# Kernel optimization log

Hardware: AMD Instinct MI355X
Metric: run time of the kernel (lower is better)

## Reference

```python
import jax, jax.numpy as jnp
import numpy as np

B, N, K, D, H = 32, 4096, 8, 256, 512
ITERS = 3
LN_EPS = 1e-5  # torch LayerNorm default; self.eps is unused in forward


def _ln(x, g, b):
    m = jnp.mean(x, axis=-1, keepdims=True)
    v = jnp.mean(jnp.square(x - m), axis=-1, keepdims=True)
    return (x - m) * jax.lax.rsqrt(v + LN_EPS) * g + b


def setup_inputs() -> dict:
    key = jax.random.key(0)
    ks = jax.random.split(key, 16)
    s = 0.02
    return {
        "inputs": jax.random.normal(ks[0], (B, N, D), jnp.float32),
        "slots_init": jax.random.normal(ks[1], (B, K, D), jnp.float32),
        "ln_in_g": jnp.ones((D,), jnp.float32), "ln_in_b": jnp.zeros((D,), jnp.float32),
        "ln_s_g": jnp.ones((D,), jnp.float32), "ln_s_b": jnp.zeros((D,), jnp.float32),
        "ln_ff_g": jnp.ones((D,), jnp.float32), "ln_ff_b": jnp.zeros((D,), jnp.float32),
        "Wk": s * jax.random.normal(ks[2], (D, D), jnp.float32), "bk": jnp.zeros((D,), jnp.float32),
        "Wq": s * jax.random.normal(ks[3], (D, D), jnp.float32), "bq": jnp.zeros((D,), jnp.float32),
        "Wv": s * jax.random.normal(ks[4], (D, D), jnp.float32), "bv": jnp.zeros((D,), jnp.float32),
        "W_ih": s * jax.random.normal(ks[5], (3 * D, D), jnp.float32),
        "b_ih": jnp.zeros((3 * D,), jnp.float32),
        "W_hh": s * jax.random.normal(ks[6], (3 * D, D), jnp.float32),
        "b_hh": jnp.zeros((3 * D,), jnp.float32),
        "W1": s * jax.random.normal(ks[7], (H, D), jnp.float32), "b1": jnp.zeros((H,), jnp.float32),
        "W2": s * jax.random.normal(ks[8], (D, H), jnp.float32), "b2": jnp.zeros((D,), jnp.float32),
    }


def _gru_cell(x, h, W_ih, b_ih, W_hh, b_hh):
    # PyTorch GRUCell: gates in order r, z, n
    gi = x @ W_ih.T + b_ih  # [*, 3D]
    gh = h @ W_hh.T + b_hh
    ir, iz, inn = jnp.split(gi, 3, axis=-1)
    hr, hz, hn = jnp.split(gh, 3, axis=-1)
    r = jax.nn.sigmoid(ir + hr)
    z = jax.nn.sigmoid(iz + hz)
    n = jnp.tanh(inn + r * hn)
    return (1.0 - z) * n + z * h


def reference(inputs, slots_init, ln_in_g, ln_in_b, ln_s_g, ln_s_b, ln_ff_g, ln_ff_b,
              Wk, bk, Wq, bq, Wv, bv, W_ih, b_ih, W_hh, b_hh, W1, b1, W2, b2):
    d = inputs.shape[-1]
    x = _ln(inputs, ln_in_g, ln_in_b)  # [B,N,D]
    # k, v depend only on x; hoisted out of the loop (same math as source)
    k = x @ Wk.T + bk                  # project_inputs
    v = x @ Wv.T + bv                  # project_v
    scale = 1.0 / jnp.sqrt(jnp.asarray(d, inputs.dtype))
    slots = slots_init
    for _ in range(ITERS):
        slots_prev = slots
        q = _ln(slots, ln_s_g, ln_s_b) @ Wq.T + bq          # [B,K,D]
        attn_logits = jnp.einsum('bkd,bnd->bkn', q, k) * scale
        # competitive softmax over the SLOT axis (dim=1), not keys
        attn = jax.nn.softmax(attn_logits, axis=1)          # [B,K,N]
        updates = jnp.einsum('bkn,bnd->bkd', attn, v)
        slots = _gru_cell(updates, slots_prev, W_ih, b_ih, W_hh, b_hh)
        hdd = jax.nn.relu(_ln(slots, ln_ff_g, ln_ff_b) @ W1.T + b1)
        slots = slots + hdd @ W2.T + b2
    return slots
```

## Files before the change

kernel.cpp:

```cpp
#include <hip/hip_runtime.h>
#include <hip/hip_bf16.h>
#include <cstddef>
#include <cstdint>

#define BB 32
#define NN 4096
#define KK 8
#define DD 256
#define HH 512
#define LN_EPS 1e-5f
#define SCALE 0.0625f
#define NCHUNK 32

__device__ __forceinline__ float wave_sum(float v) {
#pragma unroll
  for (int off = 32; off >= 1; off >>= 1) v += __shfl_xor(v, off);
  return v;
}

__device__ __forceinline__ float sigmoidf_(float x) { return 1.0f / (1.0f + __expf(-x)); }

#define OFF_G   0
#define OFF_W1  393216
#define OFF_W2  524288
#define OFF_WV  655360
#define OFF_WQ  720896
#define OFF_WK  786432
#define WB_ELEMS 851968

#define G_PRE (BB * KK)
#define G_W2B (512 * 11)
#define G_SETUP (G_PRE + G_W2B)

__device__ __forceinline__ float dotp4(uint2 w, float4 s) {
  return __uint_as_float(w.x << 16) * s.x + __uint_as_float(w.x & 0xffff0000u) * s.y +
         __uint_as_float(w.y << 16) * s.z + __uint_as_float(w.y & 0xffff0000u) * s.w;
}

template <int OUT, int KL>
__device__ __forceinline__ float gemv_p(const ushort* __restrict__ wt, int j, int kb,
                                        const float* __restrict__ src) {
  const uint2* p = (const uint2*)(wt + ((size_t)(kb >> 2) * OUT + j) * 4);
  float a = 0.0f;
#pragma unroll 16
  for (int e = 0; e < KL / 4; ++e) {
    uint2 w = p[(size_t)e * OUT];
    float4 s = *(const float4*)(src + kb + e * 4);
    a += dotp4(w, s);
  }
  return a;
}

__global__ __launch_bounds__(256) void k_setup(
    const float* __restrict__ Wih, const float* __restrict__ Whh,
    const float* __restrict__ W1, const float* __restrict__ W2,
    const float* __restrict__ Wv, const float* __restrict__ Wq,
    const float* __restrict__ Wk, ushort* __restrict__ wb,
    const float* __restrict__ slots, const float* __restrict__ gs, const float* __restrict__ bs,
    const float* __restrict__ bq, const float* __restrict__ bk,
    float* __restrict__ qk, float* __restrict__ qb) {
  int blk = blockIdx.x;
  if (blk < G_PRE) {
    int row = blk;
    int t = threadIdx.x;
    int wid = t >> 6, lane = t & 63;
    __shared__ float lns[DD];
    __shared__ float qs[DD];
    __shared__ float rb[8];
    float sv = slots[(size_t)row * DD + t];
    float s = wave_sum(sv);
    float s2 = wave_sum(sv * sv);
    if (lane == 0) { rb[wid] = s; rb[4 + wid] = s2; }
    __syncthreads();
    float tot = rb[0] + rb[1] + rb[2] + rb[3];
    float tot2 = rb[4] + rb[5] + rb[6] + rb[7];
    float m = tot * (1.0f / DD);
    float var = tot2 * (1.0f / DD) - m * m;
    float rs = rsqrtf(var + LN_EPS);
    lns[t] = (sv - m) * rs * gs[t] + bs[t];
    __syncthreads();
    float acc = 0.0f;
    const float4* wr = (const float4*)(Wq + (size_t)t * DD);
#pragma unroll 4
    for (int e4 = 0; e4 < DD / 4; ++e4) {
      float4 w = wr[e4];
      float4 l = ((const float4*)lns)[e4];
      acc += w.x * l.x + w.y * l.y + w.z * l.z + w.w * l.w;
    }
    qs[t] = acc + bq[t];
    __syncthreads();
    float a2 = 0.0f;
    for (int d = 0; d < DD; ++d) a2 = fmaf(qs[d], Wk[(size_t)d * DD + t], a2);
    qk[(size_t)row * DD + t] = SCALE * a2;
    float pb = wave_sum(qs[t] * bk[t]);
    __syncthreads();
    if (lane == 0) rb[wid] = pb;
    __syncthreads();
    if (t == 0) qb[row] = SCALE * (rb[0] + rb[1] + rb[2] + rb[3]);
  } else {
    int q2 = blk - G_PRE;
    int m = q2 >> 9;
    int idx = (q2 & 511) * 256 + threadIdx.x;
    const int sizes[11] = {65536, 65536, 65536, 65536, 65536, 65536, 131072, 131072, 65536, 65536, 65536};
    const int offs[11] = {OFF_G, OFF_G + 65536, OFF_G + 131072, OFF_G + 196608, OFF_G + 262144,
                          OFF_G + 327680, OFF_W1, OFF_W2, OFF_WV, OFF_WQ, OFF_WK};
    if (idx >= sizes[m]) return;
    int K = (m == 7) ? 512 : 256;
    int OUT = (m == 6) ? 512 : 256;
    int k = idx % K, j = idx / K;
    float v;
    switch (m) {
      case 0: case 1: case 2: v = Wih[((size_t)(m * 256 + j)) * 256 + k]; break;
      case 3: case 4: case 5: v = Whh[((size_t)((m - 3) * 256 + j)) * 256 + k]; break;
      case 6: v = W1[(size_t)j * 256 + k]; break;
      case 7: v = W2[(size_t)j * 512 + k]; break;
      case 8: v = Wv[(size_t)j * 256 + k]; break;
      case 9: v = Wq[(size_t)j * 256 + k]; break;
      default: v = Wk[(size_t)k * 256 + j]; break;
    }
    __hip_bfloat16 h = __float2bfloat16(v);
    wb[(size_t)offs[m] + (size_t)(k >> 2) * OUT * 4 + j * 4 + (k & 3)] = *(ushort*)&h;
  }
}

template <int DO_LN>
__global__ __launch_bounds__(256) void k_attn_t(const ushort* __restrict__ xb_in,
                                                ushort* __restrict__ xb_out,
                                                const float* __restrict__ inp,
                                                const float* __restrict__ lg,
                                                const float* __restrict__ lb,
                                                const float* __restrict__ qk,
                                                const float* __restrict__ qb,
                                                float* __restrict__ uxp,
                                                float* __restrict__ sap) {
  int wid = threadIdx.x >> 6, lane = threadIdx.x & 63;
  int wg = blockIdx.x * 4 + wid;
  int b = wg >> 7, wc = wg & 127;
  int l32 = lane & 31, half = lane >> 5;
  int d0 = l32 * 8;
  __shared__ float bx[KK][DD];
  __shared__ float sred[4][KK];
  float4 qa[8], qc[8];
  {
    const float* base = qk + (size_t)b * (KK * DD) + d0;
#pragma unroll
    for (int k = 0; k < 8; ++k) {
      qa[k] = *(const float4*)(base + k * DD);
      qc[k] = *(const float4*)(base + k * DD + 4);
    }
  }
  int km = ((lane & 1) << 2) | (lane & 2) | ((lane >> 2) & 1);
  float qb_mine = qb[b * 8 + km];
  float g8[8], b8[8];
  const float* rp;
  ushort* wp;
  const uint4* px;
  uint4 xv;
  if (DO_LN) {
#pragma unroll
    for (int j = 0; j < 8; ++j) { g8[j] = lg[d0 + j]; b8[j] = lb[d0 + j]; }
    rp = inp + ((size_t)b * NN + wc * 32 + half) * DD + d0;
    wp = xb_out + ((size_t)b * NN + wc * 32 + half) * DD + d0;
  } else {
    px = (const uint4*)(xb_in + ((size_t)b * NN + wc * 32 + half) * DD + d0);
    xv = px[0];
  }
  float4 ac0[8] = {}, ac1[8] = {};
  float sacc = 0.0f;
#pragma unroll 2
  for (int it = 0; it < 16; ++it) {
    float xf[8];
    if (DO_LN) {
      float4 v0 = *(const float4*)rp;
      float4 v1 = *(const float4*)(rp + 4);
      float s = v0.x + v0.y + v0.z + v0.w + v1.x + v1.y + v1.z + v1.w;
      float s2 = v0.x * v0.x + v0.y * v0.y + v0.z * v0.z + v0.w * v0.w +
                 v1.x * v1.x + v1.y * v1.y + v1.z * v1.z + v1.w * v1.w;
#pragma unroll
      for (int off = 16; off >= 1; off >>= 1) {
        s += __shfl_xor(s, off);
        s2 += __shfl_xor(s2, off);
      }
      float m = s * (1.0f / DD);
      float var = s2 * (1.0f / DD) - m * m;
      float rs = rsqrtf(var + LN_EPS);
      xf[0] = (v0.x - m) * rs * g8[0] + b8[0];
      xf[1] = (v0.y - m) * rs * g8[1] + b8[1];
      xf[2] = (v0.z - m) * rs * g8[2] + b8[2];
      xf[3] = (v0.w - m) * rs * g8[3] + b8[3];
      xf[4] = (v1.x - m) * rs * g8[4] + b8[4];
      xf[5] = (v1.y - m) * rs * g8[5] + b8[5];
      xf[6] = (v1.z - m) * rs * g8[6] + b8[6];
      xf[7] = (v1.w - m) * rs * g8[7] + b8[7];
      uint4 st;
      {
        __hip_bfloat16 h0 = __float2bfloat16(xf[0]), h1 = __float2bfloat16(xf[1]);
        __hip_bfloat16 h2 = __float2bfloat16(xf[2]), h3 = __float2bfloat16(xf[3]);
        __hip_bfloat16 h4 = __float2bfloat16(xf[4]), h5 = __float2bfloat16(xf[5]);
        __hip_bfloat16 h6 = __float2bfloat16(xf[6]), h7 = __float2bfloat16(xf[7]);
        st.x = (uint)*(ushort*)&h0 | ((uint)*(ushort*)&h1 << 16);
        st.y = (uint)*(ushort*)&h2 | ((uint)*(ushort*)&h3 << 16);
        st.z = (uint)*(ushort*)&h4 | ((uint)*(ushort*)&h5 << 16);
        st.w = (uint)*(ushort*)&h6 | ((uint)*(ushort*)&h7 << 16);
      }
      *(uint4*)wp = st;
      rp += 2 * DD;
      wp += 2 * DD;
    } else {
      uint4 nx = (it < 15) ? px[(size_t)(it + 1) * 64] : xv;
      xf[0] = __uint_as_float(xv.x << 16); xf[1] = __uint_as_float(xv.x & 0xffff0000u);
      xf[2] = __uint_as_float(xv.y << 16); xf[3] = __uint_as_float(xv.y & 0xffff0000u);
      xf[4] = __uint_as_float(xv.z << 16); xf[5] = __uint_as_float(xv.z & 0xffff0000u);
      xf[6] = __uint_as_float(xv.w << 16); xf[7] = __uint_as_float(xv.w & 0xffff0000u);
      xv = nx;
    }
    float l[8];
#pragma unroll
    for (int k = 0; k < 8; ++k) {
      l[k] = xf[0] * qa[k].x + xf[1] * qa[k].y + xf[2] * qa[k].z + xf[3] * qa[k].w +
             xf[4] * qc[k].x + xf[5] * qc[k].y + xf[6] * qc[k].z + xf[7] * qc[k].w;
    }
#pragma unroll
    for (int i = 0; i < 4; ++i) {
      float keep = (lane & 1) ? l[i + 4] : l[i];
      float send = (lane & 1) ? l[i] : l[i + 4];
      l[i] = keep + __shfl_xor(send, 1);
    }
#pragma unroll
    for (int i = 0; i < 2; ++i) {
      float keep = (lane & 2) ? l[i + 2] : l[i];
      float send = (lane & 2) ? l[i] : l[i + 2];
      l[i] = keep + __shfl_xor(send, 2);
    }
    {
      float keep = (lane & 4) ? l[1] : l[0];
      float send = (lane & 4) ? l[0] : l[1];
      l[0] = keep + __shfl_xor(send, 4);
    }
    float lv = l[0] + __shfl_xor(l[0], 8);
    lv += __shfl_xor(lv, 16);
    lv += qb_mine;
    float mx = fmaxf(lv, __shfl_xor(lv, 1));
    mx = fmaxf(mx, __shfl_xor(mx, 2));
    mx = fmaxf(mx, __shfl_xor(mx, 4));
    float p = __expf(lv - mx);
    float ss = p + __shfl_xor(p, 1);
    ss += __shfl_xor(ss, 2);
    ss += __shfl_xor(ss, 4);
    float a = p * __frcp_rn(ss);
    sacc += a;
    float ga[8];
    ga[0] = a;
    ga[1] = __shfl_xor(ga[0], 1);
    ga[2] = __shfl_xor(ga[0], 2);
    ga[3] = __shfl_xor(ga[1], 2);
    ga[4] = __shfl_xor(ga[0], 4);
    ga[5] = __shfl_xor(ga[1], 4);
    ga[6] = __shfl_xor(ga[2], 4);
    ga[7] = __shfl_xor(ga[3], 4);
#pragma unroll
    for (int j = 0; j < 8; ++j) {
      float aj = ga[j];
      ac0[j].x = fmaf(aj, xf[0], ac0[j].x);
      ac0[j].y = fmaf(aj, xf[1], ac0[j].y);
      ac0[j].z = fmaf(aj, xf[2], ac0[j].z);
      ac0[j].w = fmaf(aj, xf[3], ac0[j].w);
      ac1[j].x = fmaf(aj, xf[4], ac1[j].x);
      ac1[j].y = fmaf(aj, xf[5], ac1[j].y);
      ac1[j].z = fmaf(aj, xf[6], ac1[j].z);
      ac1[j].w = fmaf(aj, xf[7], ac1[j].w);
    }
  }
#pragma unroll
  for (int j = 0; j < 8; ++j) {
    ac0[j].x += __shfl_xor(ac0[j].x, 32);
    ac0[j].y += __shfl_xor(ac0[j].y, 32);
    ac0[j].z += __shfl_xor(ac0[j].z, 32);
    ac0[j].w += __shfl_xor(ac0[j].w, 32);
    ac1[j].x += __shfl_xor(ac1[j].x, 32);
    ac1[j].y += __shfl_xor(ac1[j].y, 32);
    ac1[j].z += __shfl_xor(ac1[j].z, 32);
    ac1[j].w += __shfl_xor(ac1[j].w, 32);
  }
  sacc += __shfl_xor(sacc, 32);
  if (lane < 8) sred[wid][km] = sacc;
#pragma unroll
  for (int w = 0; w < 4; ++w) {
    if (wid == w && half == 0) {
#pragma unroll
      for (int j = 0; j < 8; ++j) {
        int lx = (l32 ^ j) & 7;
        int kj = ((lx & 1) << 2) | (lx & 2) | ((lx >> 2) & 1);
        float4* p0 = (float4*)&bx[kj][d0];
        float4* p1 = (float4*)&bx[kj][d0 + 4];
        if (w == 0) {
          *p0 = ac0[j];
          *p1 = ac1[j];
        } else {
          float4 c0 = *p0, c1 = *p1;
          c0.x += ac0[j].x; c0.y += ac0[j].y; c0.z += ac0[j].z; c0.w += ac0[j].w;
          c1.x += ac1[j].x; c1.y += ac1[j].y; c1.z += ac1[j].z; c1.w += ac1[j].w;
          *p0 = c0; *p1 = c1;
        }
      }
    }
    __syncthreads();
  }
  int bb2 = blockIdx.x >> 5, c = blockIdx.x & 31;
  {
    int t = threadIdx.x;
    int k = t >> 5, dd = (t & 31) * 8;
    float* dst = uxp + (((size_t)(bb2 * NCHUNK + c)) * KK + k) * DD + dd;
    *(float4*)dst = *(float4*)&bx[k][dd];
    *(float4*)(dst + 4) = *(float4*)&bx[k][dd + 4];
    if (t < 8)
      sap[((size_t)(bb2 * NCHUNK + c)) * KK + t] =
          sred[0][t] + sred[1][t] + sred[2][t] + sred[3][t];
  }
}

__global__ __launch_bounds__(1024) void k_fused(const float* __restrict__ slots_in,
                                                const float* __restrict__ uxp,
                                                const float* __restrict__ sap,
                                                const ushort* __restrict__ wb,
                                                const float* __restrict__ bv,
                                                const float* __restrict__ bih, const float* __restrict__ bhh,
                                                const float* __restrict__ gff, const float* __restrict__ bff,
                                                const float* __restrict__ b1, const float* __restrict__ b2,
                                                const float* __restrict__ gs, const float* __restrict__ bs,
                                                const float* __restrict__ bq, const float* __restrict__ bk,
                                                float* __restrict__ dst,
                                                float* __restrict__ qk_out,
                                                float* __restrict__ qb_out,
                                                int last) {
  const ushort* WG = wb + OFF_G;
  const ushort* W1p = wb + OFF_W1;
  const ushort* W2p = wb + OFF_W2;
  const ushort* WVp = wb + OFF_WV;
  const ushort* WQp = wb + OFF_WQ;
  const ushort* WKp = wb + OFF_WK;

  __shared__ float ux_s[DD], h_s[DD], upd_s[DD], hn_s[DD], ln_s[DD];
  __shared__ float g_s[6][DD];
  __shared__ float hdd_s[HH];
  __shared__ float tmp4_s[4][DD];
  __shared__ float red_s[16];
  __shared__ float sA_s;
  float* tmpH = &tmp4_s[0][0];

  int t = threadIdx.x, d = t & 255, qr = t >> 8;
  int wid = t >> 6, lane = t & 63;
  int r = blockIdx.x, b = r >> 3, k = r & 7;

  {
    const float* p = uxp + (((size_t)(b * NCHUNK + qr * 8)) * KK + k) * DD + d;
    float s = 0.0f;
#pragma unroll
    for (int i = 0; i < 8; ++i) s += p[(size_t)i * KK * DD];
    tmp4_s[qr][d] = s;
  }
  if (t < 256) h_s[t] = slots_in[(size_t)r * DD + t];
  if (t >= 960) {
    int c = t - 960;
    float v = (c < NCHUNK) ? sap[((size_t)(b * NCHUNK + c)) * KK + k] : 0.0f;
    v = wave_sum(v);
    if (lane == 0) sA_s = v;
  }
  __syncthreads();
  if (t < 256) ux_s[t] = tmp4_s[0][t] + tmp4_s[1][t] + tmp4_s[2][t] + tmp4_s[3][t];
  __syncthreads();

  tmp4_s[qr][d] = gemv_p<256, 64>(WVp, d, qr * 64, ux_s);
  __syncthreads();
  if (t < 256) upd_s[t] = tmp4_s[0][t] + tmp4_s[1][t] + tmp4_s[2][t] + tmp4_s[3][t] + bv[t] * sA_s;
  __syncthreads();

  {
    int g = qr;
    const float* src = (g < 3) ? upd_s : h_s;
    float a = gemv_p<256, 256>(WG + (size_t)g * 65536, d, 0, src);
    g_s[g][d] = a + ((g < 3) ? bih[g * 256 + d] : bhh[d]);
    if (t < 512) {
      int g2 = 4 + (t >> 8), j2 = t & 255;
      float a2 = gemv_p<256, 256>(WG + (size_t)g2 * 65536, j2, 0, h_s);
      g_s[g2][j2] = a2 + bhh[(g2 - 3) * 256 + j2];
    }
  }
  __syncthreads();
  if (t < 256) {
    float rr = sigmoidf_(g_s[0][t] + g_s[3][t]);
    float zz = sigmoidf_(g_s[1][t] + g_s[4][t]);
    float nn = tanhf(g_s[2][t] + rr * g_s[5][t]);
    hn_s[t] = (1.0f - zz) * nn + zz * h_s[t];
  }
  __syncthreads();

  if (t < 256) {
    float v = hn_s[t];
    float sm = wave_sum(v), sq = wave_sum(v * v);
    if (lane == 0) { red_s[wid] = sm; red_s[8 + wid] = sq; }
  }
  __syncthreads();
  if (t < 256) {
    float v = hn_s[t];
    float tot = red_s[0] + red_s[1] + red_s[2] + red_s[3];
    float tot2 = red_s[8] + red_s[9] + red_s[10] + red_s[11];
    float m = tot * (1.0f / DD);
    float var = tot2 * (1.0f / DD) - m * m;
    float rs = rsqrtf(var + LN_EPS);
    ln_s[t] = (v - m) * rs * gff[t] + bff[t];
  }
  __syncthreads();

  {
    int o = t & 511, kh = t >> 9;
    tmpH[kh * 512 + o] = gemv_p<512, 128>(W1p, o, kh * 128, ln_s);
  }
  __syncthreads();
  if (t < 512) hdd_s[t] = fmaxf(tmpH[t] + tmpH[512 + t] + b1[t], 0.0f);
  __syncthreads();

  tmp4_s[qr][d] = gemv_p<256, 128>(W2p, d, qr * 128, hdd_s);
  __syncthreads();
  if (t < 256) {
    float o = hn_s[t] + tmp4_s[0][t] + tmp4_s[1][t] + tmp4_s[2][t] + tmp4_s[3][t] + b2[t];
    dst[(size_t)r * DD + t] = o;
    ux_s[t] = o;
  }
  __syncthreads();

  if (!last) {
    if (t < 256) {
      float v = ux_s[t];
      float sm = wave_sum(v), sq = wave_sum(v * v);
      if (lane == 0) { red_s[wid] = sm; red_s[8 + wid] = sq; }
    }
    __syncthreads();
    if (t < 256) {
      float v = ux_s[t];
      float tot = red_s[0] + red_s[1] + red_s[2] + red_s[3];
      float tot2 = red_s[8] + red_s[9] + red_s[10] + red_s[11];
      float m = tot * (1.0f / DD);
      float var = tot2 * (1.0f / DD) - m * m;
      float rs = rsqrtf(var + LN_EPS);
      ln_s[t] = (v - m) * rs * gs[t] + bs[t];
    }
    __syncthreads();
    tmp4_s[qr][d] = gemv_p<256, 64>(WQp, d, qr * 64, ln_s);
    __syncthreads();
    if (t < 256) {
      float qv = tmp4_s[0][t] + tmp4_s[1][t] + tmp4_s[2][t] + tmp4_s[3][t] + bq[t];
      upd_s[t] = qv;
      float sb = wave_sum(qv * bk[t]);
      if (lane == 0) red_s[wid] = sb;
    }
    __syncthreads();
    {
      float a = gemv_p<256, 64>(WKp, d, qr * 64, upd_s);
      tmp4_s[qr][d] = a;
    }
    __syncthreads();
    if (t < 256) qk_out[(size_t)r * DD + t] =
        SCALE * (tmp4_s[0][t] + tmp4_s[1][t] + tmp4_s[2][t] + tmp4_s[3][t]);
    if (t == 0) qb_out[r] = SCALE * (red_s[0] + red_s[1] + red_s[2] + red_s[3]);
  }
}

extern "C" void kernel_launch(void* const* d_in, const int* in_sizes, int n_in,
                              void* d_out, int out_size, void* d_ws, size_t ws_size,
                              hipStream_t stream) {
  const float* inputs = (const float*)d_in[0];
  const float* slots_init = (const float*)d_in[1];
  const float* ln_in_g = (const float*)d_in[2];
  const float* ln_in_b = (const float*)d_in[3];
  const float* ln_s_g = (const float*)d_in[4];
  const float* ln_s_b = (const float*)d_in[5];
  const float* ln_ff_g = (const float*)d_in[6];
  const float* ln_ff_b = (const float*)d_in[7];
  const float* Wk = (const float*)d_in[8];
  const float* bk = (const float*)d_in[9];
  const float* Wq = (const float*)d_in[10];
  const float* bq = (const float*)d_in[11];
  const float* Wv = (const float*)d_in[12];
  const float* bv = (const float*)d_in[13];
  const float* Wih = (const float*)d_in[14];
  const float* bih = (const float*)d_in[15];
  const float* Whh = (const float*)d_in[16];
  const float* bhh = (const float*)d_in[17];
  const float* W1 = (const float*)d_in[18];
  const float* b1 = (const float*)d_in[19];
  const float* W2 = (const float*)d_in[20];
  const float* b2 = (const float*)d_in[21];
  float* outp = (float*)d_out;

  char* w = (char*)d_ws;
  ushort* xb = (ushort*)w;       w += (size_t)BB * NN * DD * 2;
  float* qk = (float*)w;         w += (size_t)BB * KK * DD * 4;
  float* qb = (float*)w;         w += (size_t)BB * KK * 4;
  float* uxp = (float*)w;        w += (size_t)BB * NCHUNK * KK * DD * 4;
  float* sap = (float*)w;        w += (size_t)BB * NCHUNK * KK * 4;
  float* slots_ws = (float*)w;   w += (size_t)BB * KK * DD * 4;
  ushort* wb = (ushort*)w;       w += (size_t)WB_ELEMS * 2;

  k_setup<<<G_SETUP, 256, 0, stream>>>(Wih, Whh, W1, W2, Wv, Wq, Wk, wb,
                                       slots_init, ln_s_g, ln_s_b, bq, bk, qk, qb);

  for (int it = 0; it < 3; ++it) {
    if (it == 0)
      k_attn_t<1><<<BB * NCHUNK, 256, 0, stream>>>(nullptr, xb, inputs, ln_in_g, ln_in_b,
                                                   qk, qb, uxp, sap);
    else
      k_attn_t<0><<<BB * NCHUNK, 256, 0, stream>>>(xb, nullptr, nullptr, nullptr, nullptr,
                                                   qk, qb, uxp, sap);
    const float* sin = (it == 0) ? slots_init : slots_ws;
    float* dst = (it == 2) ? outp : slots_ws;
    k_fused<<<BB * KK, 1024, 0, stream>>>(sin, uxp, sap, wb,
                                          bv, bih, bhh, ln_ff_g, ln_ff_b, b1, b2,
                                          ln_s_g, ln_s_b, bq, bk,
                                          dst, qk, qb, (it == 2) ? 1 : 0);
  }
}
```

Baseline: 254.7 us.

## Stage input tiles in swizzled LDS and fold input LayerNorm affine into weights

The attention kernel now stages each wave's 32-row tile of normalized inputs in XOR-swizzled shared memory. In later iterations the tile is loaded with global_load_lds, and logits and the weighted value sums are computed from LDS, replacing the earlier register shuffle-heavy scheme. The input LayerNorm gain and bias are folded algebraically into qk/qb and into Wv and a precomputed value bias, so the stored x is just the standardized value. This cuts shuffle traffic and per-element affine work in exchange for heavy LDS use (about 72KB per block), which may lower occupancy.

Measured after the change: 264.7 us. 1.04x slower.

```diff
diff --git a/kernel.cpp b/kernel.cpp
--- a/kernel.cpp
+++ b/kernel.cpp
@@ -20,6 +20,9 @@
 
 __device__ __forceinline__ float sigmoidf_(float x) { return 1.0f / (1.0f + __expf(-x)); }
 
+__device__ __forceinline__ float bflo(uint u) { return __uint_as_float(u << 16); }
+__device__ __forceinline__ float bfhi(uint u) { return __uint_as_float(u & 0xffff0000u); }
+
 #define OFF_G   0
 #define OFF_W1  393216
 #define OFF_W2  524288
@@ -30,7 +33,7 @@
 
 #define G_PRE (BB * KK)
 #define G_W2B (512 * 11)
-#define G_SETUP (G_PRE + G_W2B)
+#define G_SETUP (G_PRE + G_W2B + 1)
 
 __device__ __forceinline__ float dotp4(uint2 w, float4 s) {
   return __uint_as_float(w.x << 16) * s.x + __uint_as_float(w.x & 0xffff0000u) * s.y +
@@ -58,6 +61,8 @@
     const float* __restrict__ Wk, ushort* __restrict__ wb,
     const float* __restrict__ slots, const float* __restrict__ gs, const float* __restrict__ bs,
     const float* __restrict__ bq, const float* __restrict__ bk,
+    const float* __restrict__ gi, const float* __restrict__ bi,
+    const float* __restrict__ bv, float* __restrict__ bvw,
     float* __restrict__ qk, float* __restrict__ qb) {
   int blk = blockIdx.x;
   if (blk < G_PRE) {
@@ -91,13 +96,15 @@
     __syncthreads();
     float a2 = 0.0f;
     for (int d = 0; d < DD; ++d) a2 = fmaf(qs[d], Wk[(size_t)d * DD + t], a2);
-    qk[(size_t)row * DD + t] = SCALE * a2;
+    float a2S = SCALE * a2;
+    qk[(size_t)row * DD + t] = a2S * gi[t];
     float pb = wave_sum(qs[t] * bk[t]);
-    __syncthreads();
-    if (lane == 0) rb[wid] = pb;
-    __syncthreads();
-    if (t == 0) qb[row] = SCALE * (rb[0] + rb[1] + rb[2] + rb[3]);
-  } else {
+    float pb2 = wave_sum(a2S * bi[t]);
+    __syncthreads();
+    if (lane == 0) { rb[wid] = pb; rb[4 + wid] = pb2; }
+    __syncthreads();
+    if (t == 0) qb[row] = SCALE * (rb[0] + rb[1] + rb[2] + rb[3]) + rb[4] + rb[5] + rb[6] + rb[7];
+  } else if (blk < G_PRE + G_W2B) {
     int q2 = blk - G_PRE;
     int m = q2 >> 9;
     int idx = (q2 & 511) * 256 + threadIdx.x;
@@ -114,12 +121,24 @@
       case 3: case 4: case 5: v = Whh[((size_t)((m - 3) * 256 + j)) * 256 + k]; break;
       case 6: v = W1[(size_t)j * 256 + k]; break;
       case 7: v = W2[(size_t)j * 512 + k]; break;
-      case 8: v = Wv[(size_t)j * 256 + k]; break;
+      case 8: v = Wv[(size_t)j * 256 + k] * gi[k]; break;
       case 9: v = Wq[(size_t)j * 256 + k]; break;
       default: v = Wk[(size_t)k * 256 + j]; break;
     }
     __hip_bfloat16 h = __float2bfloat16(v);
     wb[(size_t)offs[m] + (size_t)(k >> 2) * OUT * 4 + j * 4 + (k & 3)] = *(ushort*)&h;
+  } else {
+    int t = threadIdx.x;
+    float a = bv[t];
+    const float4* wr = (const float4*)(Wv + (size_t)t * DD);
+    const float4* bb = (const float4*)bi;
+#pragma unroll 4
+    for (int e4 = 0; e4 < DD / 4; ++e4) {
+      float4 w = wr[e4];
+      float4 x = bb[e4];
+      a += w.x * x.x + w.y * x.y + w.z * x.z + w.w * x.w;
+    }
+    bvw[t] = a;
   }
 }
 
@@ -127,196 +146,171 @@
 __global__ __launch_bounds__(256) void k_attn_t(const ushort* __restrict__ xb_in,
                                                 ushort* __restrict__ xb_out,
                                                 const float* __restrict__ inp,
-                                                const float* __restrict__ lg,
-                                                const float* __restrict__ lb,
                                                 const float* __restrict__ qk,
                                                 const float* __restrict__ qb,
                                                 float* __restrict__ uxp,
                                                 float* __restrict__ sap) {
-  int wid = threadIdx.x >> 6, lane = threadIdx.x & 63;
-  int wg = blockIdx.x * 4 + wid;
-  int b = wg >> 7, wc = wg & 127;
-  int l32 = lane & 31, half = lane >> 5;
-  int d0 = l32 * 8;
-  __shared__ float bx[KK][DD];
+  __shared__ __align__(16) float q_s[KK][DD];
+  __shared__ __align__(16) ushort xt[4][32 * DD];
+  __shared__ __align__(16) float a_s[4][KK][32];
   __shared__ float sred[4][KK];
-  float4 qa[8], qc[8];
-  {
-    const float* base = qk + (size_t)b * (KK * DD) + d0;
-#pragma unroll
-    for (int k = 0; k < 8; ++k) {
-      qa[k] = *(const float4*)(base + k * DD);
-      qc[k] = *(const float4*)(base + k * DD + 4);
-    }
-  }
-  int km = ((lane & 1) << 2) | (lane & 2) | ((lane >> 2) & 1);
-  float qb_mine = qb[b * 8 + km];
-  float g8[8], b8[8];
-  const float* rp;
-  ushort* wp;
-  const uint4* px;
-  uint4 xv;
+
+  int t = threadIdx.x, wid = t >> 6, lane = t & 63;
+  int bI = blockIdx.x >> 5, c = blockIdx.x & 31;
+  int row0 = c * 128 + wid * 32;
+  ushort* xw = xt[wid];
+
+#pragma unroll
+  for (int s = 0; s < KK; ++s) q_s[s][t] = qk[(size_t)bI * (KK * DD) + s * DD + t];
+  float qbv[KK];
+#pragma unroll
+  for (int s = 0; s < KK; ++s) qbv[s] = qb[bI * KK + s];
+  __syncthreads();
+
+  int r = lane & 31, h = lane >> 5;
+
   if (DO_LN) {
-#pragma unroll
-    for (int j = 0; j < 8; ++j) { g8[j] = lg[d0 + j]; b8[j] = lb[d0 + j]; }
-    rp = inp + ((size_t)b * NN + wc * 32 + half) * DD + d0;
-    wp = xb_out + ((size_t)b * NN + wc * 32 + half) * DD + d0;
-  } else {
-    px = (const uint4*)(xb_in + ((size_t)b * NN + wc * 32 + half) * DD + d0);
-    xv = px[0];
-  }
-  float4 ac0[8] = {}, ac1[8] = {};
-  float sacc = 0.0f;
-#pragma unroll 2
-  for (int it = 0; it < 16; ++it) {
-    float xf[8];
-    if (DO_LN) {
-      float4 v0 = *(const float4*)rp;
-      float4 v1 = *(const float4*)(rp + 4);
-      float s = v0.x + v0.y + v0.z + v0.w + v1.x + v1.y + v1.z + v1.w;
-      float s2 = v0.x * v0.x + v0.y * v0.y + v0.z * v0.z + v0.w * v0.w +
-                 v1.x * v1.x + v1.y * v1.y + v1.z * v1.z + v1.w * v1.w;
-#pragma unroll
-      for (int off = 16; off >= 1; off >>= 1) {
-        s += __shfl_xor(s, off);
-        s2 += __shfl_xor(s2, off);
+    int q8 = lane & 7, lr = lane >> 3;
+    const float* rp0 = inp + ((size_t)bI * NN + row0 + lr) * DD + q8 * 4;
+    float4 cur[8];
+#pragma unroll
+    for (int i = 0; i < 8; ++i) cur[i] = *(const float4*)(rp0 + i * 32);
+    for (int p = 0; p < 4; ++p) {
+      float4 nxt[8];
+      if (p < 3) {
+#pragma unroll
+        for (int i = 0; i < 8; ++i) nxt[i] = *(const float4*)(rp0 + (size_t)(p + 1) * 8 * DD + i * 32);
       }
-      float m = s * (1.0f / DD);
+      float s1 = 0.0f, s2 = 0.0f;
+#pragma unroll
+      for (int i = 0; i < 8; ++i) {
+        s1 += cur[i].x + cur[i].y + cur[i].z + cur[i].w;
+        s2 += cur[i].x * cur[i].x + cur[i].y * cur[i].y + cur[i].z * cur[i].z + cur[i].w * cur[i].w;
+      }
+      s1 += __shfl_xor(s1, 1); s2 += __shfl_xor(s2, 1);
+      s1 += __shfl_xor(s1, 2); s2 += __shfl_xor(s2, 2);
+      s1 += __shfl_xor(s1, 4); s2 += __shfl_xor(s2, 4);
+      float m = s1 * (1.0f / DD);
       float var = s2 * (1.0f / DD) - m * m;
       float rs = rsqrtf(var + LN_EPS);
-      xf[0] = (v0.x - m) * rs * g8[0] + b8[0];
-      xf[1] = (v0.y - m) * rs * g8[1] + b8[1];
-      xf[2] = (v0.z - m) * rs * g8[2] + b8[2];
-      xf[3] = (v0.w - m) * rs * g8[3] + b8[3];
-      xf[4] = (v1.x - m) * rs * g8[4] + b8[4];
-      xf[5] = (v1.y - m) * rs * g8[5] + b8[5];
-      xf[6] = (v1.z - m) * rs * g8[6] + b8[6];
-      xf[7] = (v1.w - m) * rs * g8[7] + b8[7];
-      uint4 st;
-      {
-        __hip_bfloat16 h0 = __float2bfloat16(xf[0]), h1 = __float2bfloat16(xf[1]);
-        __hip_bfloat16 h2 = __float2bfloat16(xf[2]), h3 = __float2bfloat16(xf[3]);
-        __hip_bfloat16 h4 = __float2bfloat16(xf[4]), h5 = __float2bfloat16(xf[5]);
-        __hip_bfloat16 h6 = __float2bfloat16(xf[6]), h7 = __float2bfloat16(xf[7]);
-        st.x = (uint)*(ushort*)&h0 | ((uint)*(ushort*)&h1 << 16);
-        st.y = (uint)*(ushort*)&h2 | ((uint)*(ushort*)&h3 << 16);
-        st.z = (uint)*(ushort*)&h4 | ((uint)*(ushort*)&h5 << 16);
-        st.w = (uint)*(ushort*)&h6 | ((uint)*(ushort*)&h7 << 16);
+      int rr = p * 8 + lr;
+      int hb = (q8 & 1) * 4;
+#pragma unroll
+      for (int i = 0; i < 8; ++i) {
+        float y0 = (cur[i].x - m) * rs, y1 = (cur[i].y - m) * rs;
+        float y2 = (cur[i].z - m) * rs, y3 = (cur[i].w - m) * rs;
+        __hip_bfloat16 h0 = __float2bfloat16(y0), h1 = __float2bfloat16(y1);
+        __hip_bfloat16 h2 = __float2bfloat16(y2), h3 = __float2bfloat16(y3);
+        uint2 wv;
+        wv.x = (uint)*(ushort*)&h0 | ((uint)*(ushort*)&h1 << 16);
+        wv.y = (uint)*(ushort*)&h2 | ((uint)*(ushort*)&h3 << 16);
+        int chunk = i * 4 + (q8 >> 1);
+        *(uint2*)&xw[rr * DD + ((chunk ^ rr) << 3) + hb] = wv;
       }
-      *(uint4*)wp = st;
-      rp += 2 * DD;
-      wp += 2 * DD;
-    } else {
-      uint4 nx = (it < 15) ? px[(size_t)(it + 1) * 64] : xv;
-      xf[0] = __uint_as_float(xv.x << 16); xf[1] = __uint_as_float(xv.x & 0xffff0000u);
-      xf[2] = __uint_as_float(xv.y << 16); xf[3] = __uint_as_float(xv.y & 0xffff0000u);
-      xf[4] = __uint_as_float(xv.z << 16); xf[5] = __uint_as_float(xv.z & 0xffff0000u);
-      xf[6] = __uint_as_float(xv.w << 16); xf[7] = __uint_as_float(xv.w & 0xffff0000u);
-      xv = nx;
-    }
-    float l[8];
-#pragma unroll
-    for (int k = 0; k < 8; ++k) {
-      l[k] = xf[0] * qa[k].x + xf[1] * qa[k].y + xf[2] * qa[k].z + xf[3] * qa[k].w +
-             xf[4] * qc[k].x + xf[5] * qc[k].y + xf[6] * qc[k].z + xf[7] * qc[k].w;
-    }
-#pragma unroll
-    for (int i = 0; i < 4; ++i) {
-      float keep = (lane & 1) ? l[i + 4] : l[i];
-      float send = (lane & 1) ? l[i] : l[i + 4];
-      l[i] = keep + __shfl_xor(send, 1);
-    }
-#pragma unroll
-    for (int i = 0; i < 2; ++i) {
-      float keep = (lane & 2) ? l[i + 2] : l[i];
-      float send = (lane & 2) ? l[i] : l[i + 2];
-      l[i] = keep + __shfl_xor(send, 2);
-    }
-    {
-      float keep = (lane & 4) ? l[1] : l[0];
-      float send = (lane & 4) ? l[0] : l[1];
-      l[0] = keep + __shfl_xor(send, 4);
-    }
-    float lv = l[0] + __shfl_xor(l[0], 8);
-    lv += __shfl_xor(lv, 16);
-    lv += qb_mine;
-    float mx = fmaxf(lv, __shfl_xor(lv, 1));
-    mx = fmaxf(mx, __shfl_xor(mx, 2));
-    mx = fmaxf(mx, __shfl_xor(mx, 4));
-    float p = __expf(lv - mx);
-    float ss = p + __shfl_xor(p, 1);
-    ss += __shfl_xor(ss, 2);
-    ss += __shfl_xor(ss, 4);
-    float a = p * __frcp_rn(ss);
-    sacc += a;
-    float ga[8];
-    ga[0] = a;
-    ga[1] = __shfl_xor(ga[0], 1);
-    ga[2] = __shfl_xor(ga[0], 2);
-    ga[3] = __shfl_xor(ga[1], 2);
-    ga[4] = __shfl_xor(ga[0], 4);
-    ga[5] = __shfl_xor(ga[1], 4);
-    ga[6] = __shfl_xor(ga[2], 4);
-    ga[7] = __shfl_xor(ga[3], 4);
-#pragma unroll
-    for (int j = 0; j < 8; ++j) {
-      float aj = ga[j];
-      ac0[j].x = fmaf(aj, xf[0], ac0[j].x);
-      ac0[j].y = fmaf(aj, xf[1], ac0[j].y);
-      ac0[j].z = fmaf(aj, xf[2], ac0[j].z);
-      ac0[j].w = fmaf(aj, xf[3], ac0[j].w);
-      ac1[j].x = fmaf(aj, xf[4], ac1[j].x);
-      ac1[j].y = fmaf(aj, xf[5], ac1[j].y);
-      ac1[j].z = fmaf(aj, xf[6], ac1[j].z);
-      ac1[j].w = fmaf(aj, xf[7], ac1[j].w);
-    }
-  }
-#pragma unroll
-  for (int j = 0; j < 8; ++j) {
-    ac0[j].x += __shfl_xor(ac0[j].x, 32);
-    ac0[j].y += __shfl_xor(ac0[j].y, 32);
-    ac0[j].z += __shfl_xor(ac0[j].z, 32);
-    ac0[j].w += __shfl_xor(ac0[j].w, 32);
-    ac1[j].x += __shfl_xor(ac1[j].x, 32);
-    ac1[j].y += __shfl_xor(ac1[j].y, 32);
-    ac1[j].z += __shfl_xor(ac1[j].z, 32);
-    ac1[j].w += __shfl_xor(ac1[j].w, 32);
-  }
-  sacc += __shfl_xor(sacc, 32);
-  if (lane < 8) sred[wid][km] = sacc;
-#pragma unroll
-  for (int w = 0; w < 4; ++w) {
-    if (wid == w && half == 0) {
-#pragma unroll
-      for (int j = 0; j < 8; ++j) {
-        int lx = (l32 ^ j) & 7;
-        int kj = ((lx & 1) << 2) | (lx & 2) | ((lx >> 2) & 1);
-        float4* p0 = (float4*)&bx[kj][d0];
-        float4* p1 = (float4*)&bx[kj][d0 + 4];
-        if (w == 0) {
-          *p0 = ac0[j];
-          *p1 = ac1[j];
-        } else {
-          float4 c0 = *p0, c1 = *p1;
-          c0.x += ac0[j].x; c0.y += ac0[j].y; c0.z += ac0[j].z; c0.w += ac0[j].w;
-          c1.x += ac1[j].x; c1.y += ac1[j].y; c1.z += ac1[j].z; c1.w += ac1[j].w;
-          *p0 = c0; *p1 = c1;
-        }
+      if (p < 3) {
+#pragma unroll
+        for (int i = 0; i < 8; ++i) cur[i] = nxt[i];
       }
     }
-    __syncthreads();
-  }
-  int bb2 = blockIdx.x >> 5, c = blockIdx.x & 31;
-  {
-    int t = threadIdx.x;
-    int k = t >> 5, dd = (t & 31) * 8;
-    float* dst = uxp + (((size_t)(bb2 * NCHUNK + c)) * KK + k) * DD + dd;
-    *(float4*)dst = *(float4*)&bx[k][dd];
-    *(float4*)(dst + 4) = *(float4*)&bx[k][dd + 4];
-    if (t < 8)
-      sap[((size_t)(bb2 * NCHUNK + c)) * KK + t] =
-          sred[0][t] + sred[1][t] + sred[2][t] + sred[3][t];
-  }
+    ushort* xbt = xb_out + ((size_t)bI * NN + row0) * DD;
+#pragma unroll
+    for (int i = 0; i < 16; ++i) {
+      uint4 v = *(const uint4*)&xw[i * 512 + lane * 8];
+      *(uint4*)&xbt[i * 512 + lane * 8] = v;
+    }
+  } else {
+    const ushort* srcb = xb_in + ((size_t)bI * NN + row0) * DD;
+#pragma unroll
+    for (int i = 0; i < 16; ++i) {
+      __builtin_amdgcn_global_load_lds(
+          (__attribute__((address_space(1))) void*)(srcb + i * 512 + lane * 8),
+          (__attribute__((address_space(3))) void*)&xw[i * 512], 16, 0, 0);
+    }
+    asm volatile("s_waitcnt vmcnt(0)" ::: "memory");
+  }
+
+  float lg[KK] = {};
+#pragma unroll 2
+  for (int m = 0; m < 16; ++m) {
+    int ch = m | (h << 4);
+    uint4 xv = *(const uint4*)&xw[r * DD + ((ch ^ r) << 3)];
+    float x0 = bflo(xv.x), x1 = bfhi(xv.x), x2 = bflo(xv.y), x3 = bfhi(xv.y);
+    float x4 = bflo(xv.z), x5 = bfhi(xv.z), x6 = bflo(xv.w), x7 = bfhi(xv.w);
+#pragma unroll
+    for (int s = 0; s < KK; ++s) {
+      const float* qp = &q_s[s][ch << 3];
+      float4 qa = *(const float4*)qp;
+      float4 qc = *(const float4*)(qp + 4);
+      lg[s] += x0 * qa.x + x1 * qa.y + x2 * qa.z + x3 * qa.w +
+               x4 * qc.x + x5 * qc.y + x6 * qc.z + x7 * qc.w;
+    }
+  }
+#pragma unroll
+  for (int s = 0; s < KK; ++s) lg[s] = lg[s] + __shfl_xor(lg[s], 32) + qbv[s];
+  float mx = lg[0];
+#pragma unroll
+  for (int s = 1; s < KK; ++s) mx = fmaxf(mx, lg[s]);
+  float a8[KK];
+  float ssum = 0.0f;
+#pragma unroll
+  for (int s = 0; s < KK; ++s) { a8[s] = __expf(lg[s] - mx); ssum += a8[s]; }
+  float rinv = __frcp_rn(ssum);
+  if (h == 0) {
+#pragma unroll
+    for (int s = 0; s < KK; ++s) a_s[wid][s][r] = a8[s] * rinv;
+  }
+
+  int s8 = lane >> 3, j = lane & 7, rot = j >> 1;
+  int kc[4];
+#pragma unroll
+  for (int cc = 0; cc < 4; ++cc) kc[cc] = 4 * j + ((cc + rot) & 3);
+  float acc[4][8] = {};
+  float sav = 0.0f;
+  for (int r4 = 0; r4 < 8; ++r4) {
+    float4 a4 = *(const float4*)&a_s[wid][s8][r4 * 4];
+#pragma unroll
+    for (int rr = 0; rr < 4; ++rr) {
+      int r2 = r4 * 4 + rr;
+      float av = (rr == 0) ? a4.x : (rr == 1) ? a4.y : (rr == 2) ? a4.z : a4.w;
+      sav += av;
+#pragma unroll
+      for (int cc = 0; cc < 4; ++cc) {
+        uint4 xv = *(const uint4*)&xw[r2 * DD + ((kc[cc] ^ r2) << 3)];
+        acc[cc][0] = fmaf(av, bflo(xv.x), acc[cc][0]);
+        acc[cc][1] = fmaf(av, bfhi(xv.x), acc[cc][1]);
+        acc[cc][2] = fmaf(av, bflo(xv.y), acc[cc][2]);
+        acc[cc][3] = fmaf(av, bfhi(xv.y), acc[cc][3]);
+        acc[cc][4] = fmaf(av, bflo(xv.z), acc[cc][4]);
+        acc[cc][5] = fmaf(av, bfhi(xv.z), acc[cc][5]);
+        acc[cc][6] = fmaf(av, bflo(xv.w), acc[cc][6]);
+        acc[cc][7] = fmaf(av, bfhi(xv.w), acc[cc][7]);
+      }
+    }
+  }
+  float* uxw = (float*)xw;
+#pragma unroll
+  for (int cc = 0; cc < 4; ++cc) {
+    float4 v0 = make_float4(acc[cc][0], acc[cc][1], acc[cc][2], acc[cc][3]);
+    float4 v1 = make_float4(acc[cc][4], acc[cc][5], acc[cc][6], acc[cc][7]);
+    *(float4*)&uxw[s8 * DD + kc[cc] * 8] = v0;
+    *(float4*)&uxw[s8 * DD + kc[cc] * 8 + 4] = v1;
+  }
+  if (j == 0) sred[wid][s8] = sav;
+  __syncthreads();
+
+  const float* x0f = (const float*)xt[0];
+  const float* x1f = (const float*)xt[1];
+  const float* x2f = (const float*)xt[2];
+  const float* x3f = (const float*)xt[3];
+  size_t obase = ((size_t)(bI * NCHUNK + c)) * (KK * DD);
+#pragma unroll
+  for (int u = 0; u < 8; ++u) {
+    int idx = u * 256 + t;
+    uxp[obase + idx] = x0f[idx] + x1f[idx] + x2f[idx] + x3f[idx];
+  }
+  if (t < 8)
+    sap[((size_t)(bI * NCHUNK + c)) * KK + t] =
+        sred[0][t] + sred[1][t] + sred[2][t] + sred[3][t];
 }
 
 __global__ __launch_bounds__(1024) void k_fused(const float* __restrict__ slots_in,
@@ -329,6 +323,7 @@
                                                 const float* __restrict__ b1, const float* __restrict__ b2,
                                                 const float* __restrict__ gs, const float* __restrict__ bs,
                                                 const float* __restrict__ bq, const float* __restrict__ bk,
+                                                const float* __restrict__ gi, const float* __restrict__ bi,
                                                 float* __restrict__ dst,
                                                 float* __restrict__ qk_out,
                                                 float* __restrict__ qb_out,
@@ -460,9 +455,15 @@
       tmp4_s[qr][d] = a;
     }
     __syncthreads();
-    if (t < 256) qk_out[(size_t)r * DD + t] =
-        SCALE * (tmp4_s[0][t] + tmp4_s[1][t] + tmp4_s[2][t] + tmp4_s[3][t]);
-    if (t == 0) qb_out[r] = SCALE * (red_s[0] + red_s[1] + red_s[2] + red_s[3]);
+    if (t < 256) {
+      float qkv = SCALE * (tmp4_s[0][t] + tmp4_s[1][t] + tmp4_s[2][t] + tmp4_s[3][t]);
+      qk_out[(size_t)r * DD + t] = qkv * gi[t];
+      float pb2 = wave_sum(qkv * bi[t]);
+      if (lane == 0) red_s[8 + wid] = pb2;
+    }
+    __syncthreads();
+    if (t == 0) qb_out[r] = SCALE * (red_s[0] + red_s[1] + red_s[2] + red_s[3]) +
+                            red_s[8] + red_s[9] + red_s[10] + red_s[11];
   }
 }
 
@@ -501,22 +502,22 @@
   float* sap = (float*)w;        w += (size_t)BB * NCHUNK * KK * 4;
   float* slots_ws = (float*)w;   w += (size_t)BB * KK * DD * 4;
   ushort* wb = (ushort*)w;       w += (size_t)WB_ELEMS * 2;
+  float* bvw = (float*)w;        w += (size_t)DD * 4;
 
   k_setup<<<G_SETUP, 256, 0, stream>>>(Wih, Whh, W1, W2, Wv, Wq, Wk, wb,
-                                       slots_init, ln_s_g, ln_s_b, bq, bk, qk, qb);
+                                       slots_init, ln_s_g, ln_s_b, bq, bk,
+                                       ln_in_g, ln_in_b, bv, bvw, qk, qb);
 
   for (int it = 0; it < 3; ++it) {
     if (it == 0)
-      k_attn_t<1><<<BB * NCHUNK, 256, 0, stream>>>(nullptr, xb, inputs, ln_in_g, ln_in_b,
-                                                   qk, qb, uxp, sap);
+      k_attn_t<1><<<BB * NCHUNK, 256, 0, stream>>>(nullptr, xb, inputs, qk, qb, uxp, sap);
     else
-      k_attn_t<0><<<BB * NCHUNK, 256, 0, stream>>>(xb, nullptr, nullptr, nullptr, nullptr,
-                                                   qk, qb, uxp, sap);
+      k_attn_t<0><<<BB * NCHUNK, 256, 0, stream>>>(xb, nullptr, nullptr, qk, qb, uxp, sap);
     const float* sin = (it == 0) ? slots_init : slots_ws;
     float* dst = (it == 2) ? outp : slots_ws;
     k_fused<<<BB * KK, 1024, 0, stream>>>(sin, uxp, sap, wb,
-                                          bv, bih, bhh, ln_ff_g, ln_ff_b, b1, b2,
-                                          ln_s_g, ln_s_b, bq, bk,
+                                          bvw, bih, bhh, ln_ff_g, ln_ff_b, b1, b2,
+                                          ln_s_g, ln_s_b, bq, bk, ln_in_g, ln_in_b,
                                           dst, qk, qb, (it == 2) ? 1 : 0);
   }
 }
```
